# Kernel tuning notes

Hardware: AMD Instinct MI355X
Metric: run time of the kernel (lower is better)

The kernel has to match this reference:

```python
import jax, jax.numpy as jnp
import numpy as np
import math

NUM_CLASSES = 15
IN_CH = 256
FEAT_CH = 256
STRIDES = (8, 16, 32, 64, 128)
SCALES = (4.0,)
RATIOS = (6.0,)
ANGLES = (-0.125 * math.pi, 0.125 * math.pi, 0.375 * math.pi, 0.625 * math.pi)
NUM_ANCHORS = len(SCALES) * len(RATIOS) * len(ANGLES)  # 4
WH_RATIO_CLIP = 1e-6


def conv2d(x, w, b, pad):
    y = jax.lax.conv_general_dilated(
        x, w, window_strides=(1, 1), padding=[(pad, pad), (pad, pad)],
        dimension_numbers=("NCHW", "OIHW", "NCHW"))
    return y + b[None, :, None, None]


def gen_grid_anchors(base_size, feat_h, feat_w, stride):
    # AnchorGeneratorRotated (S2ANet style): base anchors [A,5] = (xc,yc,w,h,angle)
    scales = jnp.asarray(SCALES, jnp.float32)
    ratios = jnp.asarray(RATIOS, jnp.float32)
    angles = jnp.asarray(ANGLES, jnp.float32)
    h_ratios = jnp.sqrt(ratios)
    w_ratios = 1.0 / h_ratios
    ones = jnp.ones_like(angles)
    ws = (base_size * w_ratios[:, None, None] * scales[None, :, None] * ones[None, None, :]).reshape(-1)
    hs = (base_size * h_ratios[:, None, None] * scales[None, :, None] * ones[None, None, :]).reshape(-1)
    ang = jnp.tile(angles, ratios.size * scales.size)
    ctr = 0.5 * (base_size - 1.0)
    base = jnp.stack([jnp.full_like(ws, ctr), jnp.full_like(ws, ctr), ws, hs, ang], axis=-1)  # [A,5]
    xx = jnp.arange(feat_w, dtype=jnp.float32) * stride
    yy = jnp.arange(feat_h, dtype=jnp.float32) * stride
    gx, gy = jnp.meshgrid(xx, yy)  # [H,W]
    zeros = jnp.zeros_like(gx)
    shift = jnp.stack([gx, gy, zeros, zeros, zeros], axis=-1)  # [H,W,5]
    return base[None, None] + shift[:, :, None, :]  # [H,W,A,5]


def norm_angle(a):
    # normalize to [-pi/4, 3pi/4)
    return (a + 0.25 * jnp.pi) % jnp.pi - 0.25 * jnp.pi


def rboxes_decode(anchors, deltas):
    # is_encode_relative=False branch of delta2rbox
    max_ratio = abs(math.log(WH_RATIO_CLIP))
    dx, dy, dw, dh, da = jnp.split(deltas, 5, axis=-1)
    rx, ry, rw, rh, ra = jnp.split(anchors, 5, axis=-1)
    dw = jnp.clip(dw, -max_ratio, max_ratio)
    dh = jnp.clip(dh, -max_ratio, max_ratio)
    gx = dx * rw + rx
    gy = dy * rh + ry
    gw = rw * jnp.exp(dw)
    gh = rh * jnp.exp(dh)
    ga = norm_angle(da + ra)
    return jnp.concatenate([gx, gy, gw, gh, ga], axis=-1)


def _head_level(x, stride, p):
    B, _, H, W = x.shape
    # reg tower (2 stacked 3x3 conv + relu)
    r = jax.nn.relu(conv2d(x, p["reg_w0"], p["reg_b0"], 1))
    r = jax.nn.relu(conv2d(r, p["reg_w1"], p["reg_b1"], 1))
    bbox = conv2d(r, p["reg_head_w"], p["reg_head_b"], 0)
    bbox = bbox.transpose(0, 2, 3, 1).reshape(B, H, W, NUM_ANCHORS, 5)
    conf = conv2d(r, p["conf_w"], p["conf_b"], 0)
    conf = conf.transpose(0, 2, 3, 1).reshape(B, H, W, NUM_ANCHORS, 1)
    anchors = gen_grid_anchors(float(stride), H, W, float(stride))  # [H,W,A,5]
    dec = rboxes_decode(anchors[None], jax.lax.stop_gradient(bbox))  # [B,H,W,A,5]
    # refine-anchor selection: pick decoded box of max-confidence anchor per location
    conf_sig = jax.nn.sigmoid(jax.lax.stop_gradient(conf))[..., 0]  # [B,H,W,A]
    idx = jnp.argmax(conf_sig, axis=3)  # [B,H,W]
    refine = jnp.take_along_axis(dec, idx[..., None, None], axis=3)[:, :, :, 0, :]  # [B,H,W,5]
    # cls tower
    c = jax.nn.relu(conv2d(x, p["cls_w0"], p["cls_b0"], 1))
    c = jax.nn.relu(conv2d(c, p["cls_w1"], p["cls_b1"], 1))
    cls = conv2d(c, p["cls_head_w"], p["cls_head_b"], 0)
    cls = cls.transpose(0, 2, 3, 1).reshape(B, H, W, NUM_ANCHORS, NUM_CLASSES)
    # per-image scores as in get_bboxes: sigmoid(cls) * sigmoid(conf)
    scores = jax.nn.sigmoid(cls.reshape(B, -1, NUM_CLASSES)) * jax.nn.sigmoid(conf.reshape(B, -1, 1))
    return scores, dec.reshape(B, -1, 5), refine


def setup_inputs() -> dict:
    key = jax.random.key(0)
    ks = jax.random.split(key, 24)
    B = 8
    sizes = [(128, 128), (64, 64), (32, 32), (16, 16), (8, 8)]
    inp = {}
    for i, (h, w) in enumerate(sizes):
        inp[f"feat{i}"] = jax.random.normal(ks[i], (B, IN_CH, h, w), jnp.float32)
    std = 0.01
    bias_cls = float(-np.log((1 - 0.01) / 0.01))
    inp["reg_w0"] = jax.random.normal(ks[5], (FEAT_CH, IN_CH, 3, 3), jnp.float32) * std
    inp["reg_b0"] = jnp.zeros((FEAT_CH,), jnp.float32)
    inp["reg_w1"] = jax.random.normal(ks[6], (FEAT_CH, FEAT_CH, 3, 3), jnp.float32) * std
    inp["reg_b1"] = jnp.zeros((FEAT_CH,), jnp.float32)
    inp["cls_w0"] = jax.random.normal(ks[7], (FEAT_CH, IN_CH, 3, 3), jnp.float32) * std
    inp["cls_b0"] = jnp.zeros((FEAT_CH,), jnp.float32)
    inp["cls_w1"] = jax.random.normal(ks[8], (FEAT_CH, FEAT_CH, 3, 3), jnp.float32) * std
    inp["cls_b1"] = jnp.zeros((FEAT_CH,), jnp.float32)
    inp["reg_head_w"] = jax.random.normal(ks[9], (5 * NUM_ANCHORS, FEAT_CH, 1, 1), jnp.float32) * std
    inp["reg_head_b"] = jnp.zeros((5 * NUM_ANCHORS,), jnp.float32)
    inp["cls_head_w"] = jax.random.normal(ks[10], (NUM_CLASSES * NUM_ANCHORS, FEAT_CH, 1, 1), jnp.float32) * std
    inp["cls_head_b"] = jnp.full((NUM_CLASSES * NUM_ANCHORS,), bias_cls, jnp.float32)
    inp["conf_w"] = jax.random.normal(ks[11], (NUM_ANCHORS, FEAT_CH, 1, 1), jnp.float32) * std
    inp["conf_b"] = jnp.full((NUM_ANCHORS,), bias_cls, jnp.float32)
    return inp


def reference(feat0, feat1, feat2, feat3, feat4,
              reg_w0, reg_b0, reg_w1, reg_b1,
              cls_w0, cls_b0, cls_w1, cls_b1,
              reg_head_w, reg_head_b, cls_head_w, cls_head_b,
              conf_w, conf_b):
    p = dict(reg_w0=reg_w0, reg_b0=reg_b0, reg_w1=reg_w1, reg_b1=reg_b1,
             cls_w0=cls_w0, cls_b0=cls_b0, cls_w1=cls_w1, cls_b1=cls_b1,
             reg_head_w=reg_head_w, reg_head_b=reg_head_b,
             cls_head_w=cls_head_w, cls_head_b=cls_head_b,
             conf_w=conf_w, conf_b=conf_b)
    feats = [feat0, feat1, feat2, feat3, feat4]
    scores_ls, boxes_ls = [], []
    for x, s in zip(feats, STRIDES):
        sc, bx, _ = _head_level(x, s, p)
        scores_ls.append(sc)
        boxes_ls.append(bx)
    scores = jnp.concatenate(scores_ls, axis=1)  # [B, N_total, num_classes]
    boxes = jnp.concatenate(boxes_ls, axis=1)    # [B, N_total, 5]
    return scores, boxes
```

## Files before the change

kernel.cpp:

```cpp
#include <hip/hip_runtime.h>


typedef __attribute__((ext_vector_type(8))) _Float16 f16x8;
typedef __attribute__((ext_vector_type(4))) float f32x4;

#define SCORES_TOTAL 10475520ull

__device__ __forceinline__ unsigned short f2h(float f) {
  union { _Float16 h; unsigned short u; } x;
  x.h = (_Float16)f;
  return x.u;
}

__device__ __forceinline__ float sigmf(float x) {
  return 1.0f / (1.0f + expf(-x));
}

__device__ __forceinline__ void gload_lds16(const unsigned short* g,
                                            unsigned short* l) {
  __builtin_amdgcn_global_load_lds(
      (const __attribute__((address_space(1))) unsigned int*)g,
      (__attribute__((address_space(3))) unsigned int*)l, 16, 0, 0);
}

__device__ __forceinline__ void lvl_lookup(int gm, int& logW, int& mbase) {
  if (gm < 131072) { logW = 7; mbase = 0; }
  else if (gm < 163840) { logW = 6; mbase = 131072; }
  else if (gm < 172032) { logW = 5; mbase = 163840; }
  else if (gm < 174080) { logW = 4; mbase = 172032; }
  else { logW = 3; mbase = 174080; }
}

__global__ __launch_bounds__(256) void prep_convw(
    const float* __restrict__ w0, const float* __restrict__ w1,
    const float* __restrict__ w2, const float* __restrict__ w3,
    unsigned short* __restrict__ wtout) {
  int g = blockIdx.x * 256 + threadIdx.x;
  int q = g >> 16;
  int wsel = q / 9;
  int kk = q - wsel * 9;
  int r = g & 65535;
  int oc = r >> 8, ic = r & 255;
  const float* src = (wsel == 0) ? w0 : (wsel == 1) ? w1 : (wsel == 2) ? w2 : w3;
  float v = src[(size_t)(oc * 256 + ic) * 9 + kk];
  wtout[(size_t)wsel * 589824 + (size_t)((kk << 8) + oc) * 256 + ic] = f2h(v);
}

__global__ __launch_bounds__(256) void prep_small(
    const float* __restrict__ clsh, const float* __restrict__ regh,
    const float* __restrict__ confw,
    unsigned short* __restrict__ wc, unsigned short* __restrict__ wh,
    unsigned short* __restrict__ zp) {
  int g = blockIdx.x * 256 + threadIdx.x;
  if (g < 16384) {
    int row = g >> 8, ic = g & 255;
    float v = (row < 60) ? clsh[row * 256 + ic] : 0.0f;
    wc[g] = f2h(v);
  } else if (g < 24576) {
    int gg = g - 16384;
    int row = gg >> 8, ic = gg & 255;
    float v = 0.0f;
    if (row < 20) v = regh[row * 256 + ic];
    else if (row < 24) v = confw[(row - 20) * 256 + ic];
    wh[gg] = f2h(v);
  } else if (g < 24640) {
    zp[g - 24576] = 0;
  }
}

__global__ __launch_bounds__(256) void to_nhwc_all(
    const float* __restrict__ f0, const float* __restrict__ f1,
    const float* __restrict__ f2, const float* __restrict__ f3,
    const float* __restrict__ f4, unsigned short* __restrict__ out) {
  __shared__ unsigned short L[64][258];
  const int t = threadIdx.x;
  const int gm0 = blockIdx.x * 64;
  int logW, mbase;
  const float* in;
  if (gm0 < 131072) { logW = 7; mbase = 0; in = f0; }
  else if (gm0 < 163840) { logW = 6; mbase = 131072; in = f1; }
  else if (gm0 < 172032) { logW = 5; mbase = 163840; in = f2; }
  else if (gm0 < 174080) { logW = 4; mbase = 172032; in = f3; }
  else { logW = 3; mbase = 174080; in = f4; }
  const int logHW = 2 * logW;
  const int HW = 1 << logHW;
  const int lm0 = gm0 - mbase;
  const int b = lm0 >> logHW;
  const int hw0 = lm0 & (HW - 1);
#pragma unroll
  for (int it = 0; it < 16; ++it) {
    int c = it * 16 + (t >> 4);
    int j4 = (t & 15) * 4;
    float4 v = *reinterpret_cast<const float4*>(
        in + (size_t)(b * 256 + c) * HW + hw0 + j4);
    L[j4 + 0][c] = f2h(v.x);
    L[j4 + 1][c] = f2h(v.y);
    L[j4 + 2][c] = f2h(v.z);
    L[j4 + 3][c] = f2h(v.w);
  }
  __syncthreads();
#pragma unroll
  for (int it = 0; it < 16; ++it) {
    int j = it * 4 + (t >> 6);
    int c4 = (t & 63) * 4;
    unsigned v0 = (unsigned)L[j][c4 + 0] | ((unsigned)L[j][c4 + 1] << 16);
    unsigned v1 = (unsigned)L[j][c4 + 2] | ((unsigned)L[j][c4 + 3] << 16);
    uint2 v = make_uint2(v0, v1);
    *reinterpret_cast<uint2*>(out + ((size_t)(gm0 + j) << 8) + c4) = v;
  }
}

__global__ __launch_bounds__(256, 2) void conv1f(
    const unsigned short* __restrict__ xin,
    const unsigned short* __restrict__ wtR,
    const unsigned short* __restrict__ wtC,
    const float* __restrict__ biasR, const float* __restrict__ biasC,
    const unsigned short* __restrict__ zp,
    unsigned short* __restrict__ outR,
    unsigned short* __restrict__ outC, int gm_base) {
  __shared__ unsigned short pool[36864];
  const int t = threadIdx.x;
  const int lane = t & 63;
  const int wv = t >> 6;
  const int wm = wv >> 1, wn = wv & 1;
  const int gm0 = gm_base + blockIdx.x * 128;
  const int n0 = blockIdx.y << 7;
  int logW, mbase;
  lvl_lookup(gm0, logW, mbase);
  const int logHW = 2 * logW;
  const int H = 1 << logW, W = H;
  const int HWm1 = (1 << logHW) - 1, Wm1 = W - 1;

  const int srow = lane >> 2;
  const int schk = (((lane & 3) ^ ((lane >> 3) & 3)) << 3);
  int hjj[2], wjj[2];
  const unsigned short* aptrj[2];
  const unsigned short* bRj[2];
  const unsigned short* bCj[2];
  const int sldrow = (wv << 5);
#pragma unroll
  for (int j = 0; j < 2; ++j) {
    int gm = gm0 + sldrow + (j << 4) + srow;
    int lm = gm - mbase;
    int hw = lm & HWm1;
    hjj[j] = hw >> logW;
    wjj[j] = hw & Wm1;
    aptrj[j] = xin + ((size_t)gm << 8) + schk;
    int br = n0 + sldrow + (j << 4) + srow;
    bRj[j] = wtR + ((size_t)br << 8) + schk;
    bCj[j] = wtC + ((size_t)br << 8) + schk;
  }

  f32x4 accR[4][4], accC[4][4];
#pragma unroll
  for (int i = 0; i < 4; ++i)
#pragma unroll
    for (int j = 0; j < 4; ++j) {
      accR[i][j] = (f32x4){0.f, 0.f, 0.f, 0.f};
      accC[i][j] = (f32x4){0.f, 0.f, 0.f, 0.f};
    }

  const int arow = (wm << 6) + (lane & 15);
  const int brow = (wn << 6) + (lane & 15);
  const int sxor = ((lane & 15) >> 1) & 3;
  const int achk = (((lane >> 4) << 3)) ^ (sxor << 3);

  auto STAGE = [&](int p, int buf) {
    int icp = p / 9;
    int kk = p - icp * 9;
    int k3 = kk / 3;
    int dy = k3 - 1, dxv = kk - k3 * 3 - 1;
    int moff = ((dy << logW) + dxv) << 8;
    int ic0 = icp << 5;
    int bko = (kk << 16) + ic0;
    const int ab = buf << 12;
#pragma unroll
    for (int j = 0; j < 2; ++j) {
      bool valid = ((unsigned)(hjj[j] + dy) < (unsigned)H) &
                   ((unsigned)(wjj[j] + dxv) < (unsigned)W);
      const unsigned short* g = valid ? (aptrj[j] + moff + ic0) : zp;
      gload_lds16(g, pool + ab + ((sldrow + (j << 4)) << 5));
    }
#pragma unroll
    for (int j = 0; j < 2; ++j) {
      gload_lds16(bRj[j] + bko, pool + 12288 + ab + ((sldrow + (j << 4)) << 5));
      gload_lds16(bCj[j] + bko, pool + 24576 + ab + ((sldrow + (j << 4)) << 5));
    }
  };

  STAGE(0, 0);
  STAGE(1, 1);

  int cbuf = 0;
#pragma unroll 1
  for (int ph = 0; ph < 72; ++ph) {
    if (ph < 71) asm volatile("s_waitcnt vmcnt(6)" ::: "memory");
    else         asm volatile("s_waitcnt vmcnt(0)" ::: "memory");
    __builtin_amdgcn_s_barrier();
    __builtin_amdgcn_sched_barrier(0);
    if (ph < 70) {
      int sb = cbuf + 2; if (sb >= 3) sb -= 3;
      STAGE(ph + 2, sb);
    }
    __builtin_amdgcn_sched_barrier(0);
    const int cb = cbuf << 12;
    f16x8 a[4], bR[4], bC[4];
#pragma unroll
    for (int mf = 0; mf < 4; ++mf)
      a[mf] = *reinterpret_cast<const f16x8*>(
          pool + cb + ((arow + (mf << 4)) << 5) + achk);
#pragma unroll
    for (int nf = 0; nf < 4; ++nf) {
      bR[nf] = *reinterpret_cast<const f16x8*>(
          pool + 12288 + cb + ((brow + (nf << 4)) << 5) + achk);
      bC[nf] = *reinterpret_cast<const f16x8*>(
          pool + 24576 + cb + ((brow + (nf << 4)) << 5) + achk);
    }
#pragma unroll
    for (int mf = 0; mf < 4; ++mf)
#pragma unroll
      for (int nf = 0; nf < 4; ++nf) {
        accR[mf][nf] = __builtin_amdgcn_mfma_f32_16x16x32_f16(
            a[mf], bR[nf], accR[mf][nf], 0, 0, 0);
        accC[mf][nf] = __builtin_amdgcn_mfma_f32_16x16x32_f16(
            a[mf], bC[nf], accC[mf][nf], 0, 0, 0);
      }
    cbuf = (cbuf == 2) ? 0 : cbuf + 1;
  }
  __syncthreads();

  const int erow = t >> 1;
  const int ech = t & 1;
  const unsigned short* esrc =
      pool + ((((erow >> 6) << 1) + ech) << 12) + ((erow & 63) << 6);
  unsigned short* ep = pool + (wv << 12);
  const int eg = (lane >> 4) << 2;
  const int el = lane & 15;
  const int lrow0 = gm0 - gm_base;

#pragma unroll
  for (int nf = 0; nf < 4; ++nf) {
    float bi = biasR[n0 + (wn << 6) + (nf << 4) + el];
#pragma unroll
    for (int mf = 0; mf < 4; ++mf)
#pragma unroll
      for (int r = 0; r < 4; ++r)
        ep[((mf << 4) + eg + r) * 64 + (nf << 4) + el] =
            f2h(fmaxf(accR[mf][nf][r] + bi, 0.0f));
  }
  __syncthreads();
  {
    unsigned short* edst =
        outR + ((size_t)(lrow0 + erow) << 8) + n0 + (ech << 6);
#pragma unroll
    for (int q = 0; q < 8; ++q)
      reinterpret_cast<uint4*>(edst)[q] =
          reinterpret_cast<const uint4*>(esrc)[q];
  }
  __syncthreads();
#pragma unroll
  for (int nf = 0; nf < 4; ++nf) {
    float bi = biasC[n0 + (wn << 6) + (nf << 4) + el];
#pragma unroll
    for (int mf = 0; mf < 4; ++mf)
#pragma unroll
      for (int r = 0; r < 4; ++r)
        ep[((mf << 4) + eg + r) * 64 + (nf << 4) + el] =
            f2h(fmaxf(accC[mf][nf][r] + bi, 0.0f));
  }
  __syncthreads();
  {
    unsigned short* edst =
        outC + ((size_t)(lrow0 + erow) << 8) + n0 + (ech << 6);
#pragma unroll
    for (int q = 0; q < 8; ++q)
      reinterpret_cast<uint4*>(edst)[q] =
          reinterpret_cast<const uint4*>(esrc)[q];
  }
}

__global__ __launch_bounds__(256, 2) void conv2w(
    const unsigned short* __restrict__ xin,
    const unsigned short* __restrict__ wt,
    const float* __restrict__ bias,
    const unsigned short* __restrict__ zp,
    unsigned short* __restrict__ yout,
    int gm_base) {
  __shared__ unsigned short pool[36864];
  const int t = threadIdx.x;
  const int lane = t & 63;
  const int wv = t >> 6;
  const int wm = wv >> 1, wn = wv & 1;
  const int gm0 = gm_base + blockIdx.x * 128;
  int logW, mbase;
  lvl_lookup(gm0, logW, mbase);
  const int logHW = 2 * logW;
  const int H = 1 << logW, W = H;
  const int HWm1 = (1 << logHW) - 1, Wm1 = W - 1;

  const int srow = lane >> 2;
  const int schk = (((lane & 3) ^ ((lane >> 3) & 3)) << 3);
  int hjj[2], wjj[2];
  const unsigned short* aptrj[2];
  const int sldrow = (wv << 5);
#pragma unroll
  for (int j = 0; j < 2; ++j) {
    int gm = gm0 + sldrow + (j << 4) + srow;
    int lm = gm - mbase;
    int hw = lm & HWm1;
    hjj[j] = hw >> logW;
    wjj[j] = hw & Wm1;
    aptrj[j] = xin + ((size_t)(gm - gm_base) << 8) + schk;
  }
  const unsigned short* bpj[4];
#pragma unroll
  for (int j = 0; j < 4; ++j) {
    int row = (wv << 6) + (j << 4) + srow;
    bpj[j] = wt + ((size_t)row << 8) + schk;
  }

  f32x4 acc[4][8];
#pragma unroll
  for (int i = 0; i < 4; ++i)
#pragma unroll
    for (int j = 0; j < 8; ++j) acc[i][j] = (f32x4){0.f, 0.f, 0.f, 0.f};

  const int arow = (wm << 6) + (lane & 15);
  const int brow = (wn << 7) + (lane & 15);
  const int sxor = ((lane & 15) >> 1) & 3;
  const int achk = (((lane >> 4) << 3)) ^ (sxor << 3);

  auto STAGE = [&](int p, int buf) {
    int icp = p / 9;
    int kk = p - icp * 9;
    int k3 = kk / 3;
    int dy = k3 - 1, dxv = kk - k3 * 3 - 1;
    int moff = ((dy << logW) + dxv) << 8;
    int ic0 = icp << 5;
    int bko = (kk << 16) + ic0;
#pragma unroll
    for (int j = 0; j < 2; ++j) {
      bool valid = ((unsigned)(hjj[j] + dy) < (unsigned)H) &
                   ((unsigned)(wjj[j] + dxv) < (unsigned)W);
      const unsigned short* g = valid ? (aptrj[j] + moff + ic0) : zp;
      gload_lds16(g, pool + (buf << 12) + ((sldrow + (j << 4)) << 5));
    }
#pragma unroll
    for (int j = 0; j < 4; ++j)
      gload_lds16(bpj[j] + bko, pool + 12288 + (buf << 13) +
                                    (((wv << 6) + (j << 4)) << 5));
  };

  STAGE(0, 0);
  STAGE(1, 1);

  int cbuf = 0;
#pragma unroll 1
  for (int ph = 0; ph < 72; ++ph) {
    if (ph < 71) asm volatile("s_waitcnt vmcnt(6)" ::: "memory");
    else         asm volatile("s_waitcnt vmcnt(0)" ::: "memory");
    __builtin_amdgcn_s_barrier();
    __builtin_amdgcn_sched_barrier(0);
    if (ph < 70) {
      int sb = cbuf + 2; if (sb >= 3) sb -= 3;
      STAGE(ph + 2, sb);
    }
    __builtin_amdgcn_sched_barrier(0);
    const int cbA = cbuf << 12;
    const int cbB = cbuf << 13;
    f16x8 a[4], b[8];
#pragma unroll
    for (int mf = 0; mf < 4; ++mf)
      a[mf] = *reinterpret_cast<const f16x8*>(
          pool + cbA + ((arow + (mf << 4)) << 5) + achk);
#pragma unroll
    for (int nf = 0; nf < 8; ++nf)
      b[nf] = *reinterpret_cast<const f16x8*>(
          pool + 12288 + cbB + ((brow + (nf << 4)) << 5) + achk);
#pragma unroll
    for (int mf = 0; mf < 4; ++mf)
#pragma unroll
      for (int nf = 0; nf < 8; ++nf)
        acc[mf][nf] = __builtin_amdgcn_mfma_f32_16x16x32_f16(
            a[mf], b[nf], acc[mf][nf], 0, 0, 0);
    cbuf = (cbuf == 2) ? 0 : cbuf + 1;
  }
  __syncthreads();

  const int erow = t >> 1;
  const int ech = t & 1;
  const unsigned short* esrc =
      pool + ((((erow >> 6) << 1) + ech) << 12) + ((erow & 63) << 6);
  unsigned short* ep = pool + (wv << 12);
  const int eg = (lane >> 4) << 2;
  const int el = lane & 15;

#pragma unroll
  for (int h = 0; h < 2; ++h) {
    if (h) __syncthreads();
#pragma unroll
    for (int q4 = 0; q4 < 4; ++q4) {
      int nf = (h << 2) + q4;
      float bi = bias[(wn << 7) + (nf << 4) + el];
#pragma unroll
      for (int mf = 0; mf < 4; ++mf)
#pragma unroll
        for (int r = 0; r < 4; ++r)
          ep[((mf << 4) + eg + r) * 64 + (q4 << 4) + el] =
              f2h(fmaxf(acc[mf][nf][r] + bi, 0.0f));
    }
    __syncthreads();
    unsigned short* edst =
        yout + ((size_t)(gm0 + erow) << 8) + (ech << 7) + (h << 6);
#pragma unroll
    for (int q = 0; q < 8; ++q)
      reinterpret_cast<uint4*>(edst)[q] =
          reinterpret_cast<const uint4*>(esrc)[q];
  }
}

__global__ __launch_bounds__(256) void head24_mfma(
    const unsigned short* __restrict__ t2,
    const unsigned short* __restrict__ wh,
    const float* __restrict__ regb, const float* __restrict__ confb,
    float* __restrict__ hbuf) {
  const int t = threadIdx.x, lane = t & 63, wv = t >> 6;
  const int rowb = blockIdx.x * 256 + wv * 64;
  const int kgrp = (lane >> 4) << 3;
  const int l15 = lane & 15;
  f32x4 acc[4][2];
#pragma unroll
  for (int i = 0; i < 4; ++i)
#pragma unroll
    for (int j = 0; j < 2; ++j) acc[i][j] = (f32x4){0.f, 0.f, 0.f, 0.f};
#pragma unroll
  for (int k0 = 0; k0 < 256; k0 += 32) {
    f16x8 a[4], b[2];
#pragma unroll
    for (int mf = 0; mf < 4; ++mf)
      a[mf] = *reinterpret_cast<const f16x8*>(
          t2 + (((size_t)(rowb + (mf << 4) + l15)) << 8) + k0 + kgrp);
#pragma unroll
    for (int nf = 0; nf < 2; ++nf)
      b[nf] = *reinterpret_cast<const f16x8*>(
          wh + (size_t)(((nf << 4) + l15) << 8) + k0 + kgrp);
#pragma unroll
    for (int mf = 0; mf < 4; ++mf)
#pragma unroll
      for (int nf = 0; nf < 2; ++nf)
        acc[mf][nf] = __builtin_amdgcn_mfma_f32_16x16x32_f16(
            a[mf], b[nf], acc[mf][nf], 0, 0, 0);
  }
#pragma unroll
  for (int nf = 0; nf < 2; ++nf) {
    int c = (nf << 4) + l15;
    if (c < 24) {
      float bi = (c < 20) ? regb[c] : confb[c - 20];
#pragma unroll
      for (int mf = 0; mf < 4; ++mf)
#pragma unroll
        for (int r = 0; r < 4; ++r) {
          int m = rowb + (mf << 4) + ((lane >> 4) << 2) + r;
          hbuf[(size_t)m * 24 + c] = acc[mf][nf][r] + bi;
        }
    }
  }
}

__global__ __launch_bounds__(256) void cls_scores(
    const unsigned short* __restrict__ t2,
    const unsigned short* __restrict__ wcw,
    const float* __restrict__ clsb,
    const float* __restrict__ hbuf,
    float* __restrict__ outs, int gm_base) {
  const int t = threadIdx.x, lane = t & 63, wv = t >> 6;
  const int gm0 = gm_base + blockIdx.x * 256;
  int logW, mbase, lvl_off;
  if (gm0 < 131072) { logW = 7; mbase = 0; lvl_off = 0; }
  else if (gm0 < 163840) { logW = 6; mbase = 131072; lvl_off = 65536; }
  else if (gm0 < 172032) { logW = 5; mbase = 163840; lvl_off = 81920; }
  else if (gm0 < 174080) { logW = 4; mbase = 172032; lvl_off = 86016; }
  else { logW = 3; mbase = 174080; lvl_off = 87040; }
  const int logHW = 2 * logW, HWm1 = (1 << logHW) - 1;
  const int rowb = gm0 + wv * 64;
  const int kgrp = (lane >> 4) << 3;
  const int l15 = lane & 15;
  f32x4 acc[4][4];
#pragma unroll
  for (int i = 0; i < 4; ++i)
#pragma unroll
    for (int j = 0; j < 4; ++j) acc[i][j] = (f32x4){0.f, 0.f, 0.f, 0.f};
#pragma unroll
  for (int k0 = 0; k0 < 256; k0 += 32) {
    f16x8 a[4], b[4];
#pragma unroll
    for (int mf = 0; mf < 4; ++mf)
      a[mf] = *reinterpret_cast<const f16x8*>(
          t2 + (((size_t)(rowb + (mf << 4) + l15)) << 8) + k0 + kgrp);
#pragma unroll
    for (int nf = 0; nf < 4; ++nf)
      b[nf] = *reinterpret_cast<const f16x8*>(
          wcw + (size_t)(((nf << 4) + l15) << 8) + k0 + kgrp);
#pragma unroll
    for (int mf = 0; mf < 4; ++mf)
#pragma unroll
      for (int nf = 0; nf < 4; ++nf)
        acc[mf][nf] = __builtin_amdgcn_mfma_f32_16x16x32_f16(
            a[mf], b[nf], acc[mf][nf], 0, 0, 0);
  }
#pragma unroll
  for (int nf = 0; nf < 4; ++nf) {
    int c = (nf << 4) + l15;
    if (c < 60) {
      int ai = c / 15, ci = c - ai * 15;
      float bi = clsb[c];
#pragma unroll
      for (int mf = 0; mf < 4; ++mf)
#pragma unroll
        for (int r = 0; r < 4; ++r) {
          int m = rowb + (mf << 4) + ((lane >> 4) << 2) + r;
          float logit = acc[mf][nf][r] + bi;
          float conf = hbuf[(size_t)m * 24 + 20 + ai];
          float sc = sigmf(logit) * sigmf(conf);
          int lm = m - mbase;
          int b = lm >> logHW;
          int hw = lm & HWm1;
          int loc = lvl_off + (hw << 2) + ai;
          outs[(size_t)b * 1309440 + (size_t)loc * 15 + ci] = sc;
        }
    }
  }
}

__global__ __launch_bounds__(256) void decode_all(
    const float* __restrict__ hbuf, float* __restrict__ outb) {
  int tid = blockIdx.x * 256 + threadIdx.x;
  if (tid >= 174592 * 4) return;
  int m = tid >> 2, a = tid & 3;
  int logW, mbase, lvl_off;
  float stride;
  if (m < 131072) { logW = 7; mbase = 0; lvl_off = 0; stride = 8.f; }
  else if (m < 163840) { logW = 6; mbase = 131072; lvl_off = 65536; stride = 16.f; }
  else if (m < 172032) { logW = 5; mbase = 163840; lvl_off = 81920; stride = 32.f; }
  else if (m < 174080) { logW = 4; mbase = 172032; lvl_off = 86016; stride = 64.f; }
  else { logW = 3; mbase = 174080; lvl_off = 87040; stride = 128.f; }
  const int logHW = 2 * logW;
  const float ANG[4] = {-0.39269908169872414f, 0.39269908169872414f,
                        1.1780972450961724f, 1.9634954084936207f};
  const float* d = hbuf + (size_t)m * 24 + a * 5;
  float dx = d[0], dy = d[1], dw = d[2], dh = d[3], da = d[4];
  int lm = m - mbase;
  int b = lm >> logHW, hw = lm & ((1 << logHW) - 1);
  int h = hw >> logW, w = hw & ((1 << logW) - 1);
  float ctr = 0.5f * (stride - 1.0f);
  float rx = w * stride + ctr, ry = h * stride + ctr;
  float rw = stride * 1.6329931618554521f;
  float rh = stride * 9.7979589711327124f;
  const float MR = 13.815510557964274f;
  dw = fminf(fmaxf(dw, -MR), MR);
  dh = fminf(fmaxf(dh, -MR), MR);
  float gx = dx * rw + rx;
  float gy = dy * rh + ry;
  float gw = rw * expf(dw);
  float gh = rh * expf(dh);
  float v = da + ANG[a] + 0.7853981633974483f;
  float r = fmodf(v, 3.14159265358979323846f);
  if (r < 0.0f) r += 3.14159265358979323846f;
  float ga = r - 0.7853981633974483f;
  int loc = lvl_off + (hw << 2) + a;
  size_t base = (size_t)b * 436480 + (size_t)loc * 5;
  outb[base + 0] = gx;
  outb[base + 1] = gy;
  outb[base + 2] = gw;
  outb[base + 3] = gh;
  outb[base + 4] = ga;
}

extern "C" void kernel_launch(void* const* d_in, const int* in_sizes, int n_in,
                              void* d_out, int out_size, void* d_ws,
                              size_t ws_size, hipStream_t stream) {
  const float* feats[5];
  for (int i = 0; i < 5; ++i) feats[i] = (const float*)d_in[i];
  const float* reg_w0 = (const float*)d_in[5];
  const float* reg_b0 = (const float*)d_in[6];
  const float* reg_w1 = (const float*)d_in[7];
  const float* reg_b1 = (const float*)d_in[8];
  const float* cls_w0 = (const float*)d_in[9];
  const float* cls_b0 = (const float*)d_in[10];
  const float* cls_w1 = (const float*)d_in[11];
  const float* cls_b1 = (const float*)d_in[12];
  const float* reg_head_w = (const float*)d_in[13];
  const float* reg_head_b = (const float*)d_in[14];
  const float* cls_head_w = (const float*)d_in[15];
  const float* cls_head_b = (const float*)d_in[16];
  const float* conf_w = (const float*)d_in[17];
  const float* conf_b = (const float*)d_in[18];

  unsigned short* ws = (unsigned short*)d_ws;
  unsigned short* t1r = ws + 44695552ull;
  unsigned short* t1c = ws + 78249984ull;
  unsigned short* wt4 = ws + 111804416ull;
  unsigned short* wh = ws + 114163712ull;
  unsigned short* wc = ws + 114171904ull;
  unsigned short* zp = ws + 114188288ull;
  float* hbuf_all = (float*)((char*)d_ws + 228376704ull);

  prep_convw<<<9216, 256, 0, stream>>>(reg_w0, reg_w1, cls_w0, cls_w1, wt4);
  prep_small<<<97, 256, 0, stream>>>(cls_head_w, reg_head_w, conf_w, wc, wh,
                                     zp);
  to_nhwc_all<<<2728, 256, 0, stream>>>(feats[0], feats[1], feats[2], feats[3],
                                        feats[4], ws);

  float* scores = (float*)d_out;
  float* boxes = (float*)d_out + SCORES_TOTAL;

  static const int gbase[2] = {0, 131072};
  static const int gM[2] = {131072, 43520};
  for (int g = 0; g < 2; ++g) {
    const int base = gbase[g];
    const int M = gM[g];
    conv1f<<<dim3(M / 128, 2), 256, 0, stream>>>(
        ws, wt4 + 0ull * 589824, wt4 + 2ull * 589824, reg_b0, cls_b0, zp, t1r,
        t1c, base);
    conv2w<<<M / 128, 256, 0, stream>>>(t1r, wt4 + 1ull * 589824, reg_b1, zp,
                                        ws, base);
    head24_mfma<<<M / 256, 256, 0, stream>>>(
        ws + ((size_t)base << 8), wh, reg_head_b, conf_b,
        hbuf_all + (size_t)base * 24);
    conv2w<<<M / 128, 256, 0, stream>>>(t1c, wt4 + 3ull * 589824, cls_b1, zp,
                                        ws, base);
    cls_scores<<<M / 256, 256, 0, stream>>>(ws, wc, cls_head_b, hbuf_all,
                                            scores, base);
  }
  decode_all<<<(174592 * 4 + 255) / 256, 256, 0, stream>>>(hbuf_all, boxes);
}
```

Measured before the change: 1.115 ms.

## Load conv weights directly from global into registers, double-buffer only activations in LDS

```diff
diff --git a/kernel.cpp b/kernel.cpp
--- a/kernel.cpp
+++ b/kernel.cpp
@@ -118,7 +118,7 @@
     const unsigned short* __restrict__ zp,
     unsigned short* __restrict__ outR,
     unsigned short* __restrict__ outC, int gm_base) {
-  __shared__ unsigned short pool[36864];
+  __shared__ unsigned short pool[16384];
   const int t = threadIdx.x;
   const int lane = t & 63;
   const int wv = t >> 6;
@@ -135,8 +135,6 @@
   const int schk = (((lane & 3) ^ ((lane >> 3) & 3)) << 3);
   int hjj[2], wjj[2];
   const unsigned short* aptrj[2];
-  const unsigned short* bRj[2];
-  const unsigned short* bCj[2];
   const int sldrow = (wv << 5);
 #pragma unroll
   for (int j = 0; j < 2; ++j) {
@@ -146,10 +144,16 @@
     hjj[j] = hw >> logW;
     wjj[j] = hw & Wm1;
     aptrj[j] = xin + ((size_t)gm << 8) + schk;
-    int br = n0 + sldrow + (j << 4) + srow;
-    bRj[j] = wtR + ((size_t)br << 8) + schk;
-    bCj[j] = wtC + ((size_t)br << 8) + schk;
-  }
+  }
+
+  const int brow = (wn << 6) + (lane & 15);
+  const int kgrp = (lane >> 4) << 3;
+  const unsigned short* wtRn = wtR + ((size_t)n0 << 8);
+  const unsigned short* wtCn = wtC + ((size_t)n0 << 8);
+  int voff[4];
+#pragma unroll
+  for (int nf = 0; nf < 4; ++nf)
+    voff[nf] = ((brow + (nf << 4)) << 8) + kgrp;
 
   f32x4 accR[4][4], accC[4][4];
 #pragma unroll
@@ -161,18 +165,16 @@
     }
 
   const int arow = (wm << 6) + (lane & 15);
-  const int brow = (wn << 6) + (lane & 15);
   const int sxor = ((lane & 15) >> 1) & 3;
-  const int achk = (((lane >> 4) << 3)) ^ (sxor << 3);
-
-  auto STAGE = [&](int p, int buf) {
+  const int achk = ((lane >> 4) ^ sxor) << 3;
+
+  auto STAGEA = [&](int p, int buf) {
     int icp = p / 9;
     int kk = p - icp * 9;
     int k3 = kk / 3;
     int dy = k3 - 1, dxv = kk - k3 * 3 - 1;
     int moff = ((dy << logW) + dxv) << 8;
     int ic0 = icp << 5;
-    int bko = (kk << 16) + ic0;
     const int ab = buf << 12;
 #pragma unroll
     for (int j = 0; j < 2; ++j) {
@@ -181,41 +183,35 @@
       const unsigned short* g = valid ? (aptrj[j] + moff + ic0) : zp;
       gload_lds16(g, pool + ab + ((sldrow + (j << 4)) << 5));
     }
-#pragma unroll
-    for (int j = 0; j < 2; ++j) {
-      gload_lds16(bRj[j] + bko, pool + 12288 + ab + ((sldrow + (j << 4)) << 5));
-      gload_lds16(bCj[j] + bko, pool + 24576 + ab + ((sldrow + (j << 4)) << 5));
-    }
   };
 
-  STAGE(0, 0);
-  STAGE(1, 1);
-
-  int cbuf = 0;
+  STAGEA(0, 0);
+  __syncthreads();
+
+  int cur = 0;
 #pragma unroll 1
   for (int ph = 0; ph < 72; ++ph) {
-    if (ph < 71) asm volatile("s_waitcnt vmcnt(6)" ::: "memory");
-    else         asm volatile("s_waitcnt vmcnt(0)" ::: "memory");
-    __builtin_amdgcn_s_barrier();
-    __builtin_amdgcn_sched_barrier(0);
-    if (ph < 70) {
-      int sb = cbuf + 2; if (sb >= 3) sb -= 3;
-      STAGE(ph + 2, sb);
-    }
-    __builtin_amdgcn_sched_barrier(0);
-    const int cb = cbuf << 12;
-    f16x8 a[4], bR[4], bC[4];
+    if (ph < 71) STAGEA(ph + 1, cur ^ 1);
+    f16x8 bR[4], bC[4];
+    {
+      int icp = ph / 9;
+      int kk = ph - icp * 9;
+      int bko = (kk << 16) + (icp << 5);
+      const unsigned short* pR = wtRn + bko;
+      const unsigned short* pC = wtCn + bko;
+#pragma unroll
+      for (int nf = 0; nf < 4; ++nf) {
+        bR[nf] = *reinterpret_cast<const f16x8*>(pR + voff[nf]);
+        bC[nf] = *reinterpret_cast<const f16x8*>(pC + voff[nf]);
+      }
+    }
+    const int cb = cur << 12;
+    f16x8 a[4];
 #pragma unroll
     for (int mf = 0; mf < 4; ++mf)
       a[mf] = *reinterpret_cast<const f16x8*>(
           pool + cb + ((arow + (mf << 4)) << 5) + achk);
-#pragma unroll
-    for (int nf = 0; nf < 4; ++nf) {
-      bR[nf] = *reinterpret_cast<const f16x8*>(
-          pool + 12288 + cb + ((brow + (nf << 4)) << 5) + achk);
-      bC[nf] = *reinterpret_cast<const f16x8*>(
-          pool + 24576 + cb + ((brow + (nf << 4)) << 5) + achk);
-    }
+    __builtin_amdgcn_s_setprio(1);
 #pragma unroll
     for (int mf = 0; mf < 4; ++mf)
 #pragma unroll
@@ -225,9 +221,10 @@
         accC[mf][nf] = __builtin_amdgcn_mfma_f32_16x16x32_f16(
             a[mf], bC[nf], accC[mf][nf], 0, 0, 0);
       }
-    cbuf = (cbuf == 2) ? 0 : cbuf + 1;
-  }
-  __syncthreads();
+    __builtin_amdgcn_s_setprio(0);
+    __syncthreads();
+    cur ^= 1;
+  }
 
   const int erow = t >> 1;
   const int ech = t & 1;
@@ -286,7 +283,7 @@
     const unsigned short* __restrict__ zp,
     unsigned short* __restrict__ yout,
     int gm_base) {
-  __shared__ unsigned short pool[36864];
+  __shared__ unsigned short pool[16384];
   const int t = threadIdx.x;
   const int lane = t & 63;
   const int wv = t >> 6;
@@ -312,12 +309,13 @@
     wjj[j] = hw & Wm1;
     aptrj[j] = xin + ((size_t)(gm - gm_base) << 8) + schk;
   }
-  const unsigned short* bpj[4];
-#pragma unroll
-  for (int j = 0; j < 4; ++j) {
-    int row = (wv << 6) + (j << 4) + srow;
-    bpj[j] = wt + ((size_t)row << 8) + schk;
-  }
+
+  const int brow = (wn << 7) + (lane & 15);
+  const int kgrp = (lane >> 4) << 3;
+  int voff[8];
+#pragma unroll
+  for (int nf = 0; nf < 8; ++nf)
+    voff[nf] = ((brow + (nf << 4)) << 8) + kgrp;
 
   f32x4 acc[4][8];
 #pragma unroll
@@ -326,66 +324,60 @@
     for (int j = 0; j < 8; ++j) acc[i][j] = (f32x4){0.f, 0.f, 0.f, 0.f};
 
   const int arow = (wm << 6) + (lane & 15);
-  const int brow = (wn << 7) + (lane & 15);
   const int sxor = ((lane & 15) >> 1) & 3;
-  const int achk = (((lane >> 4) << 3)) ^ (sxor << 3);
-
-  auto STAGE = [&](int p, int buf) {
+  const int achk = ((lane >> 4) ^ sxor) << 3;
+
+  auto STAGEA = [&](int p, int buf) {
     int icp = p / 9;
     int kk = p - icp * 9;
     int k3 = kk / 3;
     int dy = k3 - 1, dxv = kk - k3 * 3 - 1;
     int moff = ((dy << logW) + dxv) << 8;
     int ic0 = icp << 5;
-    int bko = (kk << 16) + ic0;
+    const int ab = buf << 12;
 #pragma unroll
     for (int j = 0; j < 2; ++j) {
       bool valid = ((unsigned)(hjj[j] + dy) < (unsigned)H) &
                    ((unsigned)(wjj[j] + dxv) < (unsigned)W);
       const unsigned short* g = valid ? (aptrj[j] + moff + ic0) : zp;
-      gload_lds16(g, pool + (buf << 12) + ((sldrow + (j << 4)) << 5));
-    }
-#pragma unroll
-    for (int j = 0; j < 4; ++j)
-      gload_lds16(bpj[j] + bko, pool + 12288 + (buf << 13) +
-                                    (((wv << 6) + (j << 4)) << 5));
+      gload_lds16(g, pool + ab + ((sldrow + (j << 4)) << 5));
+    }
   };
 
-  STAGE(0, 0);
-  STAGE(1, 1);
-
-  int cbuf = 0;
+  STAGEA(0, 0);
+  __syncthreads();
+
+  int cur = 0;
 #pragma unroll 1
   for (int ph = 0; ph < 72; ++ph) {
-    if (ph < 71) asm volatile("s_waitcnt vmcnt(6)" ::: "memory");
-    else         asm volatile("s_waitcnt vmcnt(0)" ::: "memory");
-    __builtin_amdgcn_s_barrier();
-    __builtin_amdgcn_sched_barrier(0);
-    if (ph < 70) {
-      int sb = cbuf + 2; if (sb >= 3) sb -= 3;
-      STAGE(ph + 2, sb);
-    }
-    __builtin_amdgcn_sched_barrier(0);
-    const int cbA = cbuf << 12;
-    const int cbB = cbuf << 13;
-    f16x8 a[4], b[8];
+    if (ph < 71) STAGEA(ph + 1, cur ^ 1);
+    f16x8 b[8];
+    {
+      int icp = ph / 9;
+      int kk = ph - icp * 9;
+      int bko = (kk << 16) + (icp << 5);
+      const unsigned short* pB = wt + bko;
+#pragma unroll
+      for (int nf = 0; nf < 8; ++nf)
+        b[nf] = *reinterpret_cast<const f16x8*>(pB + voff[nf]);
+    }
+    const int cb = cur << 12;
+    f16x8 a[4];
 #pragma unroll
     for (int mf = 0; mf < 4; ++mf)
       a[mf] = *reinterpret_cast<const f16x8*>(
-          pool + cbA + ((arow + (mf << 4)) << 5) + achk);
-#pragma unroll
-    for (int nf = 0; nf < 8; ++nf)
-      b[nf] = *reinterpret_cast<const f16x8*>(
-          pool + 12288 + cbB + ((brow + (nf << 4)) << 5) + achk);
+          pool + cb + ((arow + (mf << 4)) << 5) + achk);
+    __builtin_amdgcn_s_setprio(1);
 #pragma unroll
     for (int mf = 0; mf < 4; ++mf)
 #pragma unroll
       for (int nf = 0; nf < 8; ++nf)
         acc[mf][nf] = __builtin_amdgcn_mfma_f32_16x16x32_f16(
             a[mf], b[nf], acc[mf][nf], 0, 0, 0);
-    cbuf = (cbuf == 2) ? 0 : cbuf + 1;
-  }
-  __syncthreads();
+    __builtin_amdgcn_s_setprio(0);
+    __syncthreads();
+    cur ^= 1;
+  }
 
   const int erow = t >> 1;
   const int ech = t & 1;
@@ -397,7 +389,7 @@
 
 #pragma unroll
   for (int h = 0; h < 2; ++h) {
-    if (h) __syncthreads();
+    __syncthreads();
 #pragma unroll
     for (int q4 = 0; q4 < 4; ++q4) {
       int nf = (h << 2) + q4;
```

Result: slower. 1.943 ms (+74.3%).
